# Optimization experiments

Hardware: AMD Instinct MI355X
Metric: run time of the kernel (lower is better)

Reference implementation:

```python
import jax, jax.numpy as jnp
import numpy as np

B, N, D, H = 2, 2048, 1024, 8
DH = D // H  # head dim = 128


def setup_inputs() -> dict:
    key = jax.random.key(0)
    k0, k1, k2 = jax.random.split(key, 3)
    s = 1.0 / np.sqrt(D).astype(np.float32)
    return {
        "x": jax.random.normal(k0, (B, N, D), dtype=jnp.float32),
        "w_qkv": jax.random.normal(k1, (3 * D, D), dtype=jnp.float32) * s,
        "b_qkv": jnp.zeros((3 * D,), dtype=jnp.float32),
        "w_o": jax.random.normal(k2, (D, D), dtype=jnp.float32) * s,
        "b_o": jnp.zeros((D,), dtype=jnp.float32),
    }


def reference(x, w_qkv, b_qkv, w_o, b_o):
    b, n, d = x.shape
    h = H
    dh = d // h
    # qkv projection (torch Linear: x @ W.T + b)
    qkv = x @ w_qkv.T + b_qkv                      # [b, n, 3d]
    # rearrange 'b n (k d h) -> k b h n d': head index is INNERMOST
    qkv = qkv.reshape(b, n, 3, dh, h)              # [b, n, k, dh, h]
    qkv = jnp.transpose(qkv, (2, 0, 4, 1, 3))      # [k, b, h, n, dh]
    q, k, v = qkv[0], qkv[1], qkv[2]
    # unnormalized attention: NO softmax between the two einsums
    attn = jnp.einsum('bhik,bhjk->bhij', q, k)     # [b, h, n, n]
    out = jnp.einsum('bhik,bhkj->bhij', attn, v)   # [b, h, n, dh]
    # rearrange 'b h n d -> b n (h d)'
    out = jnp.transpose(out, (0, 2, 1, 3)).reshape(b, n, d)
    return out @ w_o.T + b_o
```

## Files before the change

### kernel.cpp

```cpp
#include <hip/hip_runtime.h>
#include <hip/hip_bf16.h>
#include <stdint.h>


typedef __bf16 bf16_t;
typedef __bf16 bf16x4 __attribute__((ext_vector_type(4)));
typedef __bf16 bf16x8 __attribute__((ext_vector_type(8)));
typedef float  fx4    __attribute__((ext_vector_type(4)));
typedef unsigned short u16;
typedef u16 u16x4 __attribute__((ext_vector_type(4)));
typedef u16 u16x8 __attribute__((ext_vector_type(8)));

typedef const void __attribute__((address_space(1)))* gas_ptr;
typedef void __attribute__((address_space(3)))*       las_ptr;

__device__ __forceinline__ void gl_lds16(const void* g, void* l) {
  __builtin_amdgcn_global_load_lds((gas_ptr)g, (las_ptr)l, 16, 0, 0);
}

#define TSLAB 262144

__global__ __launch_bounds__(256) void beacon_kernel(float* out, float val, int n)
{
  const int i = blockIdx.x * 256 + threadIdx.x;
  if (i < n) out[i] = val;
}

__global__ __launch_bounds__(256) void conv_all_kernel(
    const float* __restrict__ x, const float* __restrict__ wq,
    const float* __restrict__ wo, const float* __restrict__ bq,
    bf16_t* __restrict__ xb, bf16_t* __restrict__ wqkvb,
    bf16_t* __restrict__ wob, float* __restrict__ bqp)
{
  const int i = blockIdx.x * 256 + threadIdx.x;
  if (i < 2097152) {
    const float* src; bf16_t* dst; int soff, doff;
    if (i < 1048576) { src = x; dst = xb; soff = i; doff = i; }
    else if (i < 1835008) {
      const int j  = i - 1048576;
      const int rp = j >> 8, g = j & 255;
      const int kk = rp >> 10, rem = rp & 1023;
      const int hh = rem >> 7,  dd = rem & 127;
      const int r  = kk * 1024 + dd * 8 + hh;
      src = wq; dst = wqkvb; soff = r * 256 + g; doff = j;
    } else {
      const int j = i - 1835008;
      src = wo; dst = wob; soff = j; doff = j;
    }
    const float4 v = ((const float4*)src)[soff];
    bf16x4 o;
    o[0] = (bf16_t)v.x; o[1] = (bf16_t)v.y; o[2] = (bf16_t)v.z; o[3] = (bf16_t)v.w;
    ((bf16x4*)dst)[doff] = o;
  } else if (i < 2097920) {
    const int j = i - 2097152;
    float4 v;
    float* pv = (float*)&v;
#pragma unroll
    for (int q = 0; q < 4; ++q) {
      const int cp = j * 4 + q;
      const int kk = cp >> 10, rem = cp & 1023;
      const int hh = rem >> 7,  dd = rem & 127;
      pv[q] = bq[kk * 1024 + dd * 8 + hh];
    }
    ((float4*)bqp)[j] = v;
  }
}

__global__ __launch_bounds__(256) void gemm1_kernel(
    const bf16_t* __restrict__ A, const bf16_t* __restrict__ Bt,
    const float* __restrict__ bias, bf16_t* __restrict__ outb)
{
  __shared__ __align__(16) short As0[128*32], As1[128*32];
  __shared__ __align__(16) short Bs0[128*32], Bs1[128*32];
  const int t    = threadIdx.x;
  const int lane = t & 63;
  const int w    = t >> 6;
  const int wr   = (w >> 1) << 6;
  const int wc   = (w & 1) << 6;
  const int lrow = lane & 15;
  const int kq   = (lane >> 4) << 3;
  const int row0 = blockIdx.y * 128;
  const int col0 = blockIdx.x * 128;

  const int i0 = t, i1 = t + 256;
  const bf16_t* a0 = A  + (size_t)(row0 + (i0 >> 2)) * 1024 + ((i0 & 3) << 3);
  const bf16_t* a1 = A  + (size_t)(row0 + (i1 >> 2)) * 1024 + ((i1 & 3) << 3);
  const bf16_t* b0 = Bt + (size_t)(col0 + (i0 >> 2)) * 1024 + ((i0 & 3) << 3);
  const bf16_t* b1 = Bt + (size_t)(col0 + (i1 >> 2)) * 1024 + ((i1 & 3) << 3);

  fx4 acc[4][4] = {};

  for (int k0 = 0; k0 < 1024; k0 += 64) {
    gl_lds16(a0 + k0,      &As0[i0 * 8]);
    gl_lds16(a1 + k0,      &As0[i1 * 8]);
    gl_lds16(b0 + k0,      &Bs0[i0 * 8]);
    gl_lds16(b1 + k0,      &Bs0[i1 * 8]);
    gl_lds16(a0 + k0 + 32, &As1[i0 * 8]);
    gl_lds16(a1 + k0 + 32, &As1[i1 * 8]);
    gl_lds16(b0 + k0 + 32, &Bs1[i0 * 8]);
    gl_lds16(b1 + k0 + 32, &Bs1[i1 * 8]);
    __syncthreads();
    {
      bf16x8 af[4], bfr[4];
#pragma unroll
      for (int i = 0; i < 4; ++i)
        af[i] = *(const bf16x8*)&As0[(wr + i*16 + lrow)*32 + kq];
#pragma unroll
      for (int j = 0; j < 4; ++j)
        bfr[j] = *(const bf16x8*)&Bs0[(wc + j*16 + lrow)*32 + kq];
#pragma unroll
      for (int i = 0; i < 4; ++i)
#pragma unroll
        for (int j = 0; j < 4; ++j)
          acc[i][j] = __builtin_amdgcn_mfma_f32_16x16x32_bf16(af[i], bfr[j], acc[i][j], 0, 0, 0);
    }
    {
      bf16x8 af[4], bfr[4];
#pragma unroll
      for (int i = 0; i < 4; ++i)
        af[i] = *(const bf16x8*)&As1[(wr + i*16 + lrow)*32 + kq];
#pragma unroll
      for (int j = 0; j < 4; ++j)
        bfr[j] = *(const bf16x8*)&Bs1[(wc + j*16 + lrow)*32 + kq];
#pragma unroll
      for (int i = 0; i < 4; ++i)
#pragma unroll
        for (int j = 0; j < 4; ++j)
          acc[i][j] = __builtin_amdgcn_mfma_f32_16x16x32_bf16(af[i], bfr[j], acc[i][j], 0, 0, 0);
    }
    __syncthreads();
  }

#pragma unroll
  for (int j = 0; j < 4; ++j) {
    const int col = col0 + wc + j*16 + lrow;
    const float bv = bias[col];
#pragma unroll
    for (int i = 0; i < 4; ++i) {
#pragma unroll
      for (int r = 0; r < 4; ++r) {
        const int row = row0 + wr + i*16 + ((lane >> 4) << 2) + r;
        outb[(size_t)row * 3072 + col] = (bf16_t)(acc[i][j][r] + bv);
      }
    }
  }
}

__global__ __launch_bounds__(256) void kt_vt_kernel(
    const bf16_t* __restrict__ qkv, bf16_t* __restrict__ Kt,
    bf16_t* __restrict__ Vt)
{
  __shared__ u16 L[64][132];
  const int t  = threadIdx.x;
  const int n0 = blockIdx.x * 64;
  const int bh = blockIdx.y >> 1, kv = blockIdx.y & 1;
  const int b  = bh >> 3, h = bh & 7;
  const u16* src = (const u16*)qkv + (size_t)(b * 2048 + n0) * 3072
                   + (1 + kv) * 1024 + h * 128;

#pragma unroll
  for (int p = 0; p < 4; ++p) {
    const int idx = t + p * 256;
    const int r = idx >> 4, g = idx & 15;
    const u16x8 v = *(const u16x8*)(src + (size_t)r * 3072 + 8 * g);
    *(u16x8*)&L[r][8 * g] = v;
  }
  __syncthreads();

  bf16_t* dstb = (kv == 0 ? Kt : Vt) + (size_t)bh * TSLAB;
#pragma unroll
  for (int p = 0; p < 4; ++p) {
    const int idx = t + p * 256;
    const int c = idx >> 3, gn = idx & 7;
    u16x8 wv;
#pragma unroll
    for (int j = 0; j < 8; ++j) wv[j] = L[8 * gn + j][c];
    *(u16x8*)(dstb + (size_t)c * 2048 + n0 + 8 * gn) = wv;
  }
}

__global__ __launch_bounds__(256) void kvt_mfma_kernel(
    const bf16_t* __restrict__ Kt, const bf16_t* __restrict__ Vt,
    float* __restrict__ Mpart2)
{
  __shared__ __align__(16) short As[128*32];
  __shared__ __align__(16) short Bs[128*32];
  const int t    = threadIdx.x;
  const int lane = t & 63;
  const int w    = t >> 6;
  const int wr   = (w >> 1) << 6;
  const int wc   = (w & 1) << 6;
  const int lrow = lane & 15;
  const int kq   = (lane >> 4) << 3;
  const int ks   = blockIdx.x;
  const int bh   = blockIdx.y;
  const bf16_t* Ab = Kt + (size_t)bh * TSLAB + ks * 256;
  const bf16_t* Bb = Vt + (size_t)bh * TSLAB + ks * 256;

  const int i0 = t, i1 = t + 256;
  const bf16_t* a0 = Ab + (size_t)(i0 >> 2) * 2048 + ((i0 & 3) << 3);
  const bf16_t* a1 = Ab + (size_t)(i1 >> 2) * 2048 + ((i1 & 3) << 3);
  const bf16_t* b0 = Bb + (size_t)(i0 >> 2) * 2048 + ((i0 & 3) << 3);
  const bf16_t* b1 = Bb + (size_t)(i1 >> 2) * 2048 + ((i1 & 3) << 3);
  short* sa0 = &As[i0 * 8]; short* sa1 = &As[i1 * 8];
  short* sb0 = &Bs[i0 * 8]; short* sb1 = &Bs[i1 * 8];

  fx4 acc[4][4] = {};

  for (int k0 = 0; k0 < 256; k0 += 32) {
    gl_lds16(a0 + k0, sa0);
    gl_lds16(a1 + k0, sa1);
    gl_lds16(b0 + k0, sb0);
    gl_lds16(b1 + k0, sb1);
    __syncthreads();
    bf16x8 af[4], bfr[4];
#pragma unroll
    for (int i = 0; i < 4; ++i)
      af[i] = *(const bf16x8*)&As[(wr + i*16 + lrow)*32 + kq];
#pragma unroll
    for (int j = 0; j < 4; ++j)
      bfr[j] = *(const bf16x8*)&Bs[(wc + j*16 + lrow)*32 + kq];
#pragma unroll
    for (int i = 0; i < 4; ++i)
#pragma unroll
      for (int j = 0; j < 4; ++j)
        acc[i][j] = __builtin_amdgcn_mfma_f32_16x16x32_bf16(af[i], bfr[j], acc[i][j], 0, 0, 0);
    __syncthreads();
  }

  float* op = Mpart2 + ((size_t)(bh * 8 + ks) << 14);
#pragma unroll
  for (int j = 0; j < 4; ++j) {
    const int col = wc + j*16 + lrow;
#pragma unroll
    for (int i = 0; i < 4; ++i) {
#pragma unroll
      for (int r = 0; r < 4; ++r) {
        const int row = wr + i*16 + ((lane >> 4) << 2) + r;
        op[(size_t)row * 128 + col] = acc[i][j][r];
      }
    }
  }
}

__global__ __launch_bounds__(256) void reduce_m2(
    const float* __restrict__ Mpart2, bf16_t* __restrict__ Mb)
{
  const int t = threadIdx.x, bh = blockIdx.y;
  const int task = blockIdx.x * 256 + t;
  const float* base = Mpart2 + ((size_t)(bh * 8) << 14) + task * 4;
  float4 s = { 0.f, 0.f, 0.f, 0.f };
#pragma unroll
  for (int ks = 0; ks < 8; ++ks) {
    const float4 v = *(const float4*)(base + ((size_t)ks << 14));
    s.x += v.x; s.y += v.y; s.z += v.z; s.w += v.w;
  }
  u16x4 wv;
  bf16_t b0 = (bf16_t)s.x; wv[0] = *(u16*)&b0;
  bf16_t b1 = (bf16_t)s.y; wv[1] = *(u16*)&b1;
  bf16_t b2 = (bf16_t)s.z; wv[2] = *(u16*)&b2;
  bf16_t b3 = (bf16_t)s.w; wv[3] = *(u16*)&b3;
  *(u16x4*)(Mb + (size_t)bh * 16384 + task * 4) = wv;
}

__global__ __launch_bounds__(256) void wprime_kernel(
    const bf16_t* __restrict__ wob, const bf16_t* __restrict__ Mb,
    bf16_t* __restrict__ Wt)
{
  __shared__ __align__(16) short As[128*32];
  __shared__ __align__(16) short Bs[64*32];
  const int t    = threadIdx.x;
  const int lane = t & 63;
  const int w    = t >> 6;
  const int wm   = w >> 1;
  const int wn   = w & 1;
  const int lrow = lane & 15;
  const int kq   = (lane >> 4) << 3;
  const int o0   = (blockIdx.x >> 1) * 128;
  const int eh   = (blockIdx.x & 1) * 64;
  const int bh   = blockIdx.y, b = bh >> 3, h = bh & 7;
  const bf16_t* A  = wob + (size_t)o0 * 1024 + h * 128;
  const bf16_t* Bt = Mb + (size_t)bh * 16384 + (size_t)eh * 128;

  const int i0 = t, i1 = t + 256;
  const bf16_t* a0 = A  + (size_t)(i0 >> 2) * 1024 + ((i0 & 3) << 3);
  const bf16_t* a1 = A  + (size_t)(i1 >> 2) * 1024 + ((i1 & 3) << 3);
  const bf16_t* b0 = Bt + (size_t)(i0 >> 2) * 128  + ((i0 & 3) << 3);
  short* sa0 = &As[i0 * 8]; short* sa1 = &As[i1 * 8];
  short* sb0 = &Bs[i0 * 8];

  fx4 acc[4][2] = {};

  for (int k0 = 0; k0 < 128; k0 += 32) {
    gl_lds16(a0 + k0, sa0);
    gl_lds16(a1 + k0, sa1);
    gl_lds16(b0 + k0, sb0);
    __syncthreads();
    bf16x8 af[4], bfr[2];
#pragma unroll
    for (int i = 0; i < 4; ++i)
      af[i] = *(const bf16x8*)&As[(wm*64 + i*16 + lrow)*32 + kq];
#pragma unroll
    for (int j = 0; j < 2; ++j)
      bfr[j] = *(const bf16x8*)&Bs[(wn*32 + j*16 + lrow)*32 + kq];
#pragma unroll
    for (int i = 0; i < 4; ++i)
#pragma unroll
      for (int j = 0; j < 2; ++j)
        acc[i][j] = __builtin_amdgcn_mfma_f32_16x16x32_bf16(af[i], bfr[j], acc[i][j], 0, 0, 0);
    __syncthreads();
  }

  bf16_t* obase = Wt + (size_t)b * 1048576 + h * 128;
#pragma unroll
  for (int j = 0; j < 2; ++j) {
    const int col = eh + wn*32 + j*16 + lrow;
#pragma unroll
    for (int i = 0; i < 4; ++i) {
#pragma unroll
      for (int r = 0; r < 4; ++r) {
        const int row = o0 + wm*64 + i*16 + ((lane >> 4) << 2) + r;
        obase[(size_t)row * 1024 + col] = (bf16_t)acc[i][j][r];
      }
    }
  }
}

__global__ __launch_bounds__(256) void gemm2_kernel(
    const bf16_t* __restrict__ A,
    const bf16_t* __restrict__ Wt,
    const float* __restrict__ bias,
    float* __restrict__ out)
{
  __shared__ __align__(16) short As0[128*32], As1[128*32];
  __shared__ __align__(16) short Bs0[64*32],  Bs1[64*32];
  const int t    = threadIdx.x;
  const int lane = t & 63;
  const int w    = t >> 6;
  const int wm   = w >> 1;
  const int wn   = w & 1;
  const int lrow = lane & 15;
  const int kq   = (lane >> 4) << 3;
  const int row0 = blockIdx.y * 128;
  const int col0 = blockIdx.x * 64;
  const bf16_t* Bt = Wt + (row0 >= 2048 ? (size_t)1048576 : (size_t)0);

  const int i0 = t, i1 = t + 256;
  const bf16_t* a0 = A  + (size_t)(row0 + (i0 >> 2)) * 3072 + ((i0 & 3) << 3);
  const bf16_t* a1 = A  + (size_t)(row0 + (i1 >> 2)) * 3072 + ((i1 & 3) << 3);
  const bf16_t* b0 = Bt + (size_t)(col0 + (i0 >> 2)) * 1024 + ((i0 & 3) << 3);

  fx4 acc[4][2] = {};

  for (int k0 = 0; k0 < 1024; k0 += 64) {
    gl_lds16(a0 + k0,      &As0[i0 * 8]);
    gl_lds16(a1 + k0,      &As0[i1 * 8]);
    gl_lds16(b0 + k0,      &Bs0[i0 * 8]);
    gl_lds16(a0 + k0 + 32, &As1[i0 * 8]);
    gl_lds16(a1 + k0 + 32, &As1[i1 * 8]);
    gl_lds16(b0 + k0 + 32, &Bs1[i0 * 8]);
    __syncthreads();
    {
      bf16x8 af[4], bfr[2];
#pragma unroll
      for (int i = 0; i < 4; ++i)
        af[i] = *(const bf16x8*)&As0[(wm*64 + i*16 + lrow)*32 + kq];
#pragma unroll
      for (int j = 0; j < 2; ++j)
        bfr[j] = *(const bf16x8*)&Bs0[(wn*32 + j*16 + lrow)*32 + kq];
#pragma unroll
      for (int i = 0; i < 4; ++i)
#pragma unroll
        for (int j = 0; j < 2; ++j)
          acc[i][j] = __builtin_amdgcn_mfma_f32_16x16x32_bf16(af[i], bfr[j], acc[i][j], 0, 0, 0);
    }
    {
      bf16x8 af[4], bfr[2];
#pragma unroll
      for (int i = 0; i < 4; ++i)
        af[i] = *(const bf16x8*)&As1[(wm*64 + i*16 + lrow)*32 + kq];
#pragma unroll
      for (int j = 0; j < 2; ++j)
        bfr[j] = *(const bf16x8*)&Bs1[(wn*32 + j*16 + lrow)*32 + kq];
#pragma unroll
      for (int i = 0; i < 4; ++i)
#pragma unroll
        for (int j = 0; j < 2; ++j)
          acc[i][j] = __builtin_amdgcn_mfma_f32_16x16x32_bf16(af[i], bfr[j], acc[i][j], 0, 0, 0);
    }
    __syncthreads();
  }

#pragma unroll
  for (int j = 0; j < 2; ++j) {
    const int col = col0 + wn*32 + j*16 + lrow;
    const float bv = bias[col];
#pragma unroll
    for (int i = 0; i < 4; ++i) {
#pragma unroll
      for (int r = 0; r < 4; ++r) {
        const int row = row0 + wm*64 + i*16 + ((lane >> 4) << 2) + r;
        out[(size_t)row * 1024 + col] = acc[i][j][r] + bv;
      }
    }
  }
}

extern "C" void kernel_launch(void* const* d_in, const int* in_sizes, int n_in,
                              void* d_out, int out_size, void* d_ws, size_t ws_size,
                              hipStream_t stream) {
  float* out = (float*)d_out;
  dim3 blk(256);

  int ix = -1, iwq = -1, ibq = -1, iwo = -1, ibo = -1;
  if (n_in == 5) {
    for (int i = 0; i < 5; ++i) {
      switch (in_sizes[i]) {
        case 4194304: ix  = i; break;
        case 3145728: iwq = i; break;
        case 3072:    ibq = i; break;
        case 1048576: iwo = i; break;
        case 1024:    ibo = i; break;
        default: break;
      }
    }
  }
  if (ix < 0 || iwq < 0 || ibq < 0 || iwo < 0 || ibo < 0) {
    beacon_kernel<<<dim3((out_size + 255) / 256), blk, 0, stream>>>(out, 50000.0f, out_size);
    return;
  }
  const size_t NEEDED = (size_t)40 * 1048576;
  if (ws_size < NEEDED) {
    beacon_kernel<<<dim3((out_size + 255) / 256), blk, 0, stream>>>(out, 30000.0f, out_size);
    return;
  }

  char* ws = (char*)d_ws;
  bf16_t* xb     = (bf16_t*)(ws);
  bf16_t* wqkvb  = (bf16_t*)(ws + (size_t)8  * 1048576);
  bf16_t* wob    = (bf16_t*)(ws + (size_t)14 * 1048576);
  bf16_t* qkv    = (bf16_t*)(ws + (size_t)16 * 1048576);
  bf16_t* Kt     = (bf16_t*)(ws);
  bf16_t* Mb     = (bf16_t*)(ws + (size_t)8  * 1048576);
  bf16_t* Wt     = (bf16_t*)(ws + (size_t)9  * 1048576);
  float*  bqp    = (float*)d_out;
  float*  Mpart2 = (float*)d_out;
  bf16_t* Vt     = (bf16_t*)d_out + 4194304;

  const float* bo = (const float*)d_in[ibo];

  conv_all_kernel<<<dim3(8195),   blk, 0, stream>>>((const float*)d_in[ix],
                                                    (const float*)d_in[iwq],
                                                    (const float*)d_in[iwo],
                                                    (const float*)d_in[ibq],
                                                    xb, wqkvb, wob, bqp);
  gemm1_kernel   <<<dim3(24, 32), blk, 0, stream>>>(xb, wqkvb, bqp, qkv);
  kt_vt_kernel   <<<dim3(32, 32), blk, 0, stream>>>(qkv, Kt, Vt);
  kvt_mfma_kernel<<<dim3(8, 16),  blk, 0, stream>>>(Kt, Vt, Mpart2);
  reduce_m2      <<<dim3(16, 16), blk, 0, stream>>>(Mpart2, Mb);
  wprime_kernel  <<<dim3(16, 16), blk, 0, stream>>>(wob, Mb, Wt);
  gemm2_kernel   <<<dim3(16, 32), blk, 0, stream>>>(qkv, Wt, bo, out);
}
```

Before: 166.6 us.

## Fuse K/V transpose into QKV GEMM epilogue and split KᵀV by head-dim halves

The QKV projection GEMM now writes Q directly in a compact layout and transposes K and V through shared memory in its epilogue, so the separate kt_vt transpose kernel and the qkv round trip are gone. The GEMM main loop drops from 64-wide double LDS stages to 32-wide single stages to make room for the transpose buffer. The KᵀV partial kernel is split across two head-dim halves, doubling its grid, and K/V buffers move into the workspace. The cost is extra syncs and LDS in the GEMM epilogue and fewer MFMAs per barrier in the main loop.

```diff
diff --git a/kernel.cpp b/kernel.cpp
--- a/kernel.cpp
+++ b/kernel.cpp
@@ -68,10 +68,12 @@
 
 __global__ __launch_bounds__(256) void gemm1_kernel(
     const bf16_t* __restrict__ A, const bf16_t* __restrict__ Bt,
-    const float* __restrict__ bias, bf16_t* __restrict__ outb)
-{
-  __shared__ __align__(16) short As0[128*32], As1[128*32];
-  __shared__ __align__(16) short Bs0[128*32], Bs1[128*32];
+    const float* __restrict__ bias, bf16_t* __restrict__ Qd,
+    bf16_t* __restrict__ Kt, bf16_t* __restrict__ Vt)
+{
+  __shared__ __align__(16) short As[128*32];
+  __shared__ __align__(16) short Bs[128*32];
+  __shared__ __align__(16) u16 LT[64][132];
   const int t    = threadIdx.x;
   const int lane = t & 63;
   const int w    = t >> 6;
@@ -87,159 +89,147 @@
   const bf16_t* a1 = A  + (size_t)(row0 + (i1 >> 2)) * 1024 + ((i1 & 3) << 3);
   const bf16_t* b0 = Bt + (size_t)(col0 + (i0 >> 2)) * 1024 + ((i0 & 3) << 3);
   const bf16_t* b1 = Bt + (size_t)(col0 + (i1 >> 2)) * 1024 + ((i1 & 3) << 3);
+  short* sa0 = &As[i0 * 8]; short* sa1 = &As[i1 * 8];
+  short* sb0 = &Bs[i0 * 8]; short* sb1 = &Bs[i1 * 8];
 
   fx4 acc[4][4] = {};
 
-  for (int k0 = 0; k0 < 1024; k0 += 64) {
-    gl_lds16(a0 + k0,      &As0[i0 * 8]);
-    gl_lds16(a1 + k0,      &As0[i1 * 8]);
-    gl_lds16(b0 + k0,      &Bs0[i0 * 8]);
-    gl_lds16(b1 + k0,      &Bs0[i1 * 8]);
-    gl_lds16(a0 + k0 + 32, &As1[i0 * 8]);
-    gl_lds16(a1 + k0 + 32, &As1[i1 * 8]);
-    gl_lds16(b0 + k0 + 32, &Bs1[i0 * 8]);
-    gl_lds16(b1 + k0 + 32, &Bs1[i1 * 8]);
-    __syncthreads();
-    {
-      bf16x8 af[4], bfr[4];
-#pragma unroll
-      for (int i = 0; i < 4; ++i)
-        af[i] = *(const bf16x8*)&As0[(wr + i*16 + lrow)*32 + kq];
+  for (int k0 = 0; k0 < 1024; k0 += 32) {
+    gl_lds16(a0 + k0, sa0);
+    gl_lds16(a1 + k0, sa1);
+    gl_lds16(b0 + k0, sb0);
+    gl_lds16(b1 + k0, sb1);
+    __syncthreads();
+    bf16x8 af[4], bfr[4];
+#pragma unroll
+    for (int i = 0; i < 4; ++i)
+      af[i] = *(const bf16x8*)&As[(wr + i*16 + lrow)*32 + kq];
+#pragma unroll
+    for (int j = 0; j < 4; ++j)
+      bfr[j] = *(const bf16x8*)&Bs[(wc + j*16 + lrow)*32 + kq];
+#pragma unroll
+    for (int i = 0; i < 4; ++i)
 #pragma unroll
       for (int j = 0; j < 4; ++j)
-        bfr[j] = *(const bf16x8*)&Bs0[(wc + j*16 + lrow)*32 + kq];
-#pragma unroll
-      for (int i = 0; i < 4; ++i)
-#pragma unroll
-        for (int j = 0; j < 4; ++j)
-          acc[i][j] = __builtin_amdgcn_mfma_f32_16x16x32_bf16(af[i], bfr[j], acc[i][j], 0, 0, 0);
-    }
-    {
-      bf16x8 af[4], bfr[4];
-#pragma unroll
-      for (int i = 0; i < 4; ++i)
-        af[i] = *(const bf16x8*)&As1[(wr + i*16 + lrow)*32 + kq];
-#pragma unroll
-      for (int j = 0; j < 4; ++j)
-        bfr[j] = *(const bf16x8*)&Bs1[(wc + j*16 + lrow)*32 + kq];
-#pragma unroll
-      for (int i = 0; i < 4; ++i)
-#pragma unroll
-        for (int j = 0; j < 4; ++j)
-          acc[i][j] = __builtin_amdgcn_mfma_f32_16x16x32_bf16(af[i], bfr[j], acc[i][j], 0, 0, 0);
-    }
-    __syncthreads();
-  }
-
-#pragma unroll
-  for (int j = 0; j < 4; ++j) {
-    const int col = col0 + wc + j*16 + lrow;
-    const float bv = bias[col];
-#pragma unroll
-    for (int i = 0; i < 4; ++i) {
-#pragma unroll
-      for (int r = 0; r < 4; ++r) {
-        const int row = row0 + wr + i*16 + ((lane >> 4) << 2) + r;
-        outb[(size_t)row * 3072 + col] = (bf16_t)(acc[i][j][r] + bv);
-      }
-    }
-  }
-}
-
-__global__ __launch_bounds__(256) void kt_vt_kernel(
-    const bf16_t* __restrict__ qkv, bf16_t* __restrict__ Kt,
-    bf16_t* __restrict__ Vt)
-{
-  __shared__ u16 L[64][132];
-  const int t  = threadIdx.x;
-  const int n0 = blockIdx.x * 64;
-  const int bh = blockIdx.y >> 1, kv = blockIdx.y & 1;
-  const int b  = bh >> 3, h = bh & 7;
-  const u16* src = (const u16*)qkv + (size_t)(b * 2048 + n0) * 3072
-                   + (1 + kv) * 1024 + h * 128;
-
-#pragma unroll
-  for (int p = 0; p < 4; ++p) {
-    const int idx = t + p * 256;
-    const int r = idx >> 4, g = idx & 15;
-    const u16x8 v = *(const u16x8*)(src + (size_t)r * 3072 + 8 * g);
-    *(u16x8*)&L[r][8 * g] = v;
-  }
-  __syncthreads();
-
-  bf16_t* dstb = (kv == 0 ? Kt : Vt) + (size_t)bh * TSLAB;
-#pragma unroll
-  for (int p = 0; p < 4; ++p) {
-    const int idx = t + p * 256;
-    const int c = idx >> 3, gn = idx & 7;
-    u16x8 wv;
-#pragma unroll
-    for (int j = 0; j < 8; ++j) wv[j] = L[8 * gn + j][c];
-    *(u16x8*)(dstb + (size_t)c * 2048 + n0 + 8 * gn) = wv;
-  }
-}
-
-__global__ __launch_bounds__(256) void kvt_mfma_kernel(
+        acc[i][j] = __builtin_amdgcn_mfma_f32_16x16x32_bf16(af[i], bfr[j], acc[i][j], 0, 0, 0);
+    __syncthreads();
+  }
+
+  const int q4 = (lane >> 4) << 2;
+  const int kk = col0 >> 10;
+
+  if (kk == 0) {
+#pragma unroll
+    for (int j = 0; j < 4; ++j) {
+      const int col = col0 + wc + j*16 + lrow;
+      const float bv = bias[col];
+#pragma unroll
+      for (int i = 0; i < 4; ++i) {
+#pragma unroll
+        for (int r = 0; r < 4; ++r) {
+          const int row = row0 + wr + i*16 + q4 + r;
+          Qd[(size_t)row * 1024 + col] = (bf16_t)(acc[i][j][r] + bv);
+        }
+      }
+    }
+  } else {
+    bf16_t* slab = (kk == 1 ? Kt : Vt)
+                 + (size_t)((row0 >> 11) * 8 + ((col0 >> 7) & 7)) * TSLAB;
+    const int n0 = row0 & 2047;
+    const int myhalf = w & 1;
+#pragma unroll
+    for (int p = 0; p < 2; ++p) {
+      if (myhalf == p) {
+#pragma unroll
+        for (int j = 0; j < 4; ++j) {
+          const int cl = j*16 + lrow;
+          const float bv = bias[col0 + p*64 + cl];
+#pragma unroll
+          for (int i = 0; i < 4; ++i) {
+            const int rb = wr + i*16 + q4;
+            u16x4 v4;
+#pragma unroll
+            for (int r = 0; r < 4; ++r) {
+              bf16_t bb = (bf16_t)(acc[i][j][r] + bv);
+              v4[r] = *(u16*)&bb;
+            }
+            *(u16x4*)&LT[cl][rb] = v4;
+          }
+        }
+      }
+      __syncthreads();
+#pragma unroll
+      for (int p2 = 0; p2 < 4; ++p2) {
+        const int t2 = t + p2 * 256;
+        const int c = t2 >> 4, g = t2 & 15;
+        const u16x4 lo = *(const u16x4*)&LT[c][8*g];
+        const u16x4 hi = *(const u16x4*)&LT[c][8*g + 4];
+        u16x8 v;
+        v[0]=lo[0]; v[1]=lo[1]; v[2]=lo[2]; v[3]=lo[3];
+        v[4]=hi[0]; v[5]=hi[1]; v[6]=hi[2]; v[7]=hi[3];
+        *(u16x8*)(slab + (size_t)(p*64 + c) * 2048 + n0 + 8*g) = v;
+      }
+      __syncthreads();
+    }
+  }
+}
+
+__global__ __launch_bounds__(256) void kvt_kernel(
     const bf16_t* __restrict__ Kt, const bf16_t* __restrict__ Vt,
     float* __restrict__ Mpart2)
 {
   __shared__ __align__(16) short As[128*32];
-  __shared__ __align__(16) short Bs[128*32];
+  __shared__ __align__(16) short Bs[64*32];
   const int t    = threadIdx.x;
   const int lane = t & 63;
   const int w    = t >> 6;
-  const int wr   = (w >> 1) << 6;
-  const int wc   = (w & 1) << 6;
+  const int wm   = w >> 1, wn = w & 1;
   const int lrow = lane & 15;
   const int kq   = (lane >> 4) << 3;
-  const int ks   = blockIdx.x;
+  const int ks   = blockIdx.x >> 1, dh = blockIdx.x & 1;
   const int bh   = blockIdx.y;
   const bf16_t* Ab = Kt + (size_t)bh * TSLAB + ks * 256;
-  const bf16_t* Bb = Vt + (size_t)bh * TSLAB + ks * 256;
+  const bf16_t* Bb = Vt + (size_t)bh * TSLAB + (size_t)(dh * 64) * 2048 + ks * 256;
 
   const int i0 = t, i1 = t + 256;
   const bf16_t* a0 = Ab + (size_t)(i0 >> 2) * 2048 + ((i0 & 3) << 3);
   const bf16_t* a1 = Ab + (size_t)(i1 >> 2) * 2048 + ((i1 & 3) << 3);
   const bf16_t* b0 = Bb + (size_t)(i0 >> 2) * 2048 + ((i0 & 3) << 3);
-  const bf16_t* b1 = Bb + (size_t)(i1 >> 2) * 2048 + ((i1 & 3) << 3);
   short* sa0 = &As[i0 * 8]; short* sa1 = &As[i1 * 8];
-  short* sb0 = &Bs[i0 * 8]; short* sb1 = &Bs[i1 * 8];
-
-  fx4 acc[4][4] = {};
+  short* sb0 = &Bs[i0 * 8];
+
+  fx4 acc[4][2] = {};
 
   for (int k0 = 0; k0 < 256; k0 += 32) {
     gl_lds16(a0 + k0, sa0);
     gl_lds16(a1 + k0, sa1);
     gl_lds16(b0 + k0, sb0);
-    gl_lds16(b1 + k0, sb1);
-    __syncthreads();
-    bf16x8 af[4], bfr[4];
-#pragma unroll
-    for (int i = 0; i < 4; ++i)
-      af[i] = *(const bf16x8*)&As[(wr + i*16 + lrow)*32 + kq];
-#pragma unroll
-    for (int j = 0; j < 4; ++j)
-      bfr[j] = *(const bf16x8*)&Bs[(wc + j*16 + lrow)*32 + kq];
-#pragma unroll
-    for (int i = 0; i < 4; ++i)
-#pragma unroll
-      for (int j = 0; j < 4; ++j)
+    __syncthreads();
+    bf16x8 af[4], bfr[2];
+#pragma unroll
+    for (int i = 0; i < 4; ++i)
+      af[i] = *(const bf16x8*)&As[(wm*64 + i*16 + lrow)*32 + kq];
+#pragma unroll
+    for (int j = 0; j < 2; ++j)
+      bfr[j] = *(const bf16x8*)&Bs[(wn*32 + j*16 + lrow)*32 + kq];
+#pragma unroll
+    for (int i = 0; i < 4; ++i)
+#pragma unroll
+      for (int j = 0; j < 2; ++j)
         acc[i][j] = __builtin_amdgcn_mfma_f32_16x16x32_bf16(af[i], bfr[j], acc[i][j], 0, 0, 0);
     __syncthreads();
   }
 
-  float* op = Mpart2 + ((size_t)(bh * 8 + ks) << 14);
-#pragma unroll
-  for (int j = 0; j < 4; ++j) {
-    const int col = wc + j*16 + lrow;
-#pragma unroll
-    for (int i = 0; i < 4; ++i) {
-#pragma unroll
-      for (int r = 0; r < 4; ++r) {
-        const int row = wr + i*16 + ((lane >> 4) << 2) + r;
-        op[(size_t)row * 128 + col] = acc[i][j][r];
-      }
-    }
+  float* op = Mpart2 + ((size_t)(bh * 8 + ks) << 14) + dh * 64;
+  const int q4 = (lane >> 4) << 2;
+#pragma unroll
+  for (int j = 0; j < 2; ++j) {
+    const int colL = wn*32 + j*16 + lrow;
+#pragma unroll
+    for (int i = 0; i < 4; ++i)
+#pragma unroll
+      for (int r = 0; r < 4; ++r)
+        op[(size_t)(wm*64 + i*16 + q4 + r) * 128 + colL] = acc[i][j][r];
   }
 }
 
@@ -346,8 +336,8 @@
   const bf16_t* Bt = Wt + (row0 >= 2048 ? (size_t)1048576 : (size_t)0);
 
   const int i0 = t, i1 = t + 256;
-  const bf16_t* a0 = A  + (size_t)(row0 + (i0 >> 2)) * 3072 + ((i0 & 3) << 3);
-  const bf16_t* a1 = A  + (size_t)(row0 + (i1 >> 2)) * 3072 + ((i1 & 3) << 3);
+  const bf16_t* a0 = A  + (size_t)(row0 + (i0 >> 2)) * 1024 + ((i0 & 3) << 3);
+  const bf16_t* a1 = A  + (size_t)(row0 + (i1 >> 2)) * 1024 + ((i1 & 3) << 3);
   const bf16_t* b0 = Bt + (size_t)(col0 + (i0 >> 2)) * 1024 + ((i0 & 3) << 3);
 
   fx4 acc[4][2] = {};
@@ -439,13 +429,13 @@
   bf16_t* xb     = (bf16_t*)(ws);
   bf16_t* wqkvb  = (bf16_t*)(ws + (size_t)8  * 1048576);
   bf16_t* wob    = (bf16_t*)(ws + (size_t)14 * 1048576);
-  bf16_t* qkv    = (bf16_t*)(ws + (size_t)16 * 1048576);
-  bf16_t* Kt     = (bf16_t*)(ws);
+  bf16_t* Qd     = (bf16_t*)(ws + (size_t)16 * 1048576);
+  bf16_t* Kt     = (bf16_t*)(ws + (size_t)24 * 1048576);
+  bf16_t* Vt     = (bf16_t*)(ws + (size_t)32 * 1048576);
   bf16_t* Mb     = (bf16_t*)(ws + (size_t)8  * 1048576);
   bf16_t* Wt     = (bf16_t*)(ws + (size_t)9  * 1048576);
   float*  bqp    = (float*)d_out;
   float*  Mpart2 = (float*)d_out;
-  bf16_t* Vt     = (bf16_t*)d_out + 4194304;
 
   const float* bo = (const float*)d_in[ibo];
 
@@ -454,10 +444,9 @@
                                                     (const float*)d_in[iwo],
                                                     (const float*)d_in[ibq],
                                                     xb, wqkvb, wob, bqp);
-  gemm1_kernel   <<<dim3(24, 32), blk, 0, stream>>>(xb, wqkvb, bqp, qkv);
-  kt_vt_kernel   <<<dim3(32, 32), blk, 0, stream>>>(qkv, Kt, Vt);
-  kvt_mfma_kernel<<<dim3(8, 16),  blk, 0, stream>>>(Kt, Vt, Mpart2);
+  gemm1_kernel   <<<dim3(24, 32), blk, 0, stream>>>(xb, wqkvb, bqp, Qd, Kt, Vt);
+  kvt_kernel     <<<dim3(16, 16), blk, 0, stream>>>(Kt, Vt, Mpart2);
   reduce_m2      <<<dim3(16, 16), blk, 0, stream>>>(Mpart2, Mb);
   wprime_kernel  <<<dim3(16, 16), blk, 0, stream>>>(wob, Mb, Wt);
-  gemm2_kernel   <<<dim3(16, 32), blk, 0, stream>>>(qkv, Wt, bo, out);
-}
+  gemm2_kernel   <<<dim3(16, 32), blk, 0, stream>>>(Qd, Wt, bo, out);
+}
```

Result: no change. 164.8 us (-1.0%).
